# Optimization experiments

Measured on AMD Instinct MI355X. Metric: run time of the kernel, lower is better.

Reference implementation:

```python
import jax, jax.numpy as jnp
import numpy as np

C = 768
H = 12
T = 4096
B = 1
EPS = 1e-5


def setup_inputs() -> dict:
    key = jax.random.key(0)
    ks = jax.random.split(key, 16)
    s = 0.02
    return {
        "x": jax.random.normal(ks[0], (B, T, C), jnp.float32),
        "ln1_w": jnp.ones((C,), jnp.float32),
        "ln1_b": jnp.zeros((C,), jnp.float32),
        "W_attn": jax.random.normal(ks[1], (C, 3 * C), jnp.float32) * s,
        "b_attn": jnp.zeros((3 * C,), jnp.float32),
        "W_proj": jax.random.normal(ks[2], (C, C), jnp.float32) * s,
        "b_proj": jnp.zeros((C,), jnp.float32),
        "ln2_w": jnp.ones((C,), jnp.float32),
        "ln2_b": jnp.zeros((C,), jnp.float32),
        "W_fc": jax.random.normal(ks[3], (C, 4 * C), jnp.float32) * s,
        "b_fc": jnp.zeros((4 * C,), jnp.float32),
        "W_fc2": jax.random.normal(ks[4], (4 * C, C), jnp.float32) * s,
        "b_fc2": jnp.zeros((C,), jnp.float32),
    }


def _layernorm(x, w, b):
    mu = jnp.mean(x, axis=-1, keepdims=True)
    var = jnp.var(x, axis=-1, keepdims=True)
    return (x - mu) * jax.lax.rsqrt(var + EPS) * w + b


def _attn(x, W_attn, b_attn, W_proj, b_proj):
    Bb, Tt, Cc = x.shape
    hd = Cc // H
    qkv = x @ W_attn + b_attn                       # (B,T,3C)
    q, k, v = jnp.split(qkv, 3, axis=-1)
    q = q.reshape(Bb, Tt, H, hd).transpose(0, 2, 1, 3)  # (B,H,T,hd)
    k = k.reshape(Bb, Tt, H, hd).transpose(0, 2, 1, 3)
    v = v.reshape(Bb, Tt, H, hd).transpose(0, 2, 1, 3)
    att = jnp.einsum('bhqd,bhkd->bhqk', q, k) * (1.0 / np.sqrt(hd))
    causal = jnp.tril(jnp.ones((Tt, Tt), bool))
    att = jnp.where(causal, att, -jnp.inf)
    att = jax.nn.softmax(att, axis=-1)
    y = jnp.einsum('bhqk,bhkd->bhqd', att, v)       # (B,H,T,hd)
    y = y.transpose(0, 2, 1, 3).reshape(Bb, Tt, Cc)
    return y @ W_proj + b_proj


def _mlp(x, W_fc, b_fc, W_fc2, b_fc2):
    h = jax.nn.gelu(x @ W_fc + b_fc, approximate=False)
    return h @ W_fc2 + b_fc2


def reference(x, ln1_w, ln1_b, W_attn, b_attn, W_proj, b_proj,
              ln2_w, ln2_b, W_fc, b_fc, W_fc2, b_fc2):
    x = x + _attn(_layernorm(x, ln1_w, ln1_b), W_attn, b_attn, W_proj, b_proj)
    x = x + _mlp(_layernorm(x, ln2_w, ln2_b), W_fc, b_fc, W_fc2, b_fc2)
    return x
```

## Files before the change

kernel.cpp:

```cpp
#include <hip/hip_runtime.h>
#include <hip/hip_bf16.h>
#include <math.h>
#include <type_traits>

#define TSEQ 4096
#define CDIM 768
#define NH 12
#define HD 64

typedef float f32x4 __attribute__((ext_vector_type(4)));
typedef __bf16 bf16x8 __attribute__((ext_vector_type(8)));
typedef short s16x8 __attribute__((ext_vector_type(8)));
typedef uint u32x4 __attribute__((ext_vector_type(4)));
typedef uint u32x2 __attribute__((ext_vector_type(2)));

__device__ inline ushort f2bf(float f) {
  __hip_bfloat16 h = __float2bfloat16(f);
  return __builtin_bit_cast(ushort, h);
}

__device__ inline void async16(const void* g, void* l) {
  __builtin_amdgcn_global_load_lds(
      (__attribute__((address_space(1))) unsigned int*)(uintptr_t)g,
      (__attribute__((address_space(3))) unsigned int*)(uintptr_t)l, 16, 0, 0);
}

__device__ inline float exp2_fast(float x) {
  float r;
  asm volatile("v_exp_f32 %0, %1\n\ts_nop 0" : "=v"(r) : "v"(x));
  return r;
}

__device__ inline uint cvtpk(float a, float b) {
  uint r;
  asm volatile("v_cvt_pk_bf16_f32 %0, %1, %2" : "=v"(r) : "v"(a), "v"(b));
  return r;
}

__device__ inline u32x4 gload16(const void* p) {
  u32x4 r;
  asm volatile("global_load_dwordx4 %0, %1, off" : "=&v"(r) : "v"(p) : "memory");
  return r;
}

__device__ inline bf16x8 frag_read(const ushort* base, int row, int kk, int lane) {
  const int byte = row * 128 + ((((kk * 4 + (lane >> 4)) ^ (row & 7))) << 4);
  return *(const bf16x8*)((const char*)base + byte);
}

__device__ inline bf16x8 frag_readK(const ushort* base, int row, int kk, int g) {
  const int f = ((row & 3) << 1) | ((row >> 3) & 1);
  const int byte = row * 128 + (((kk * 4 + g) ^ f) << 4);
  return *(const bf16x8*)((const char*)base + byte);
}

__device__ void wconv_body(const float* __restrict__ W, ushort* __restrict__ Wt,
                           int K, int N, int bx, int by)
{
  __shared__ float sm[32][33];
  const int n0 = bx * 32, k0 = by * 32;
  const int c = threadIdx.x & 31, r0 = threadIdx.x >> 5;
#pragma unroll
  for (int i = 0; i < 4; ++i) {
    const int r = r0 + i * 8;
    sm[r][c] = W[(size_t)(k0 + r) * N + n0 + c];
  }
  __syncthreads();
#pragma unroll
  for (int i = 0; i < 4; ++i) {
    const int r = r0 + i * 8;
    Wt[(size_t)(n0 + r) * K + k0 + c] = f2bf(sm[c][r]);
  }
}

__device__ void ln_body(const float* __restrict__ x, const float* __restrict__ w,
                        const float* __restrict__ b, ushort* __restrict__ out, int row)
{
  const int tid = threadIdx.x;
  const float* xr = x + (size_t)row * CDIM;
  float v[3];
  float s1 = 0.f, s2 = 0.f;
#pragma unroll
  for (int i = 0; i < 3; ++i) {
    v[i] = xr[tid + i * 256];
    s1 += v[i];
    s2 += v[i] * v[i];
  }
#pragma unroll
  for (int off = 32; off >= 1; off >>= 1) {
    s1 += __shfl_xor(s1, off, 64);
    s2 += __shfl_xor(s2, off, 64);
  }
  __shared__ float red1[4], red2[4];
  if ((tid & 63) == 0) { red1[tid >> 6] = s1; red2[tid >> 6] = s2; }
  __syncthreads();
  s1 = red1[0] + red1[1] + red1[2] + red1[3];
  s2 = red2[0] + red2[1] + red2[2] + red2[3];
  const float mu = s1 * (1.f / CDIM);
  const float var = s2 * (1.f / CDIM) - mu * mu;
  const float inv = rsqrtf(var + 1e-5f);
#pragma unroll
  for (int i = 0; i < 3; ++i) {
    const int c2 = tid + i * 256;
    out[(size_t)row * CDIM + c2] = f2bf((v[i] - mu) * inv * w[c2] + b[c2]);
  }
}

__global__ __launch_bounds__(256) void prep_kernel(
    const float* __restrict__ W_attn, ushort* __restrict__ Wt_attn,
    const float* __restrict__ W_proj, ushort* __restrict__ Wt_proj,
    const float* __restrict__ W_fc,   ushort* __restrict__ Wt_fc,
    const float* __restrict__ W_fc2,  ushort* __restrict__ Wt_fc2,
    const float* __restrict__ x, const float* __restrict__ ln1w,
    const float* __restrict__ ln1b, ushort* __restrict__ t_ln)
{
  int b = blockIdx.x;
  if (b < 1728) { wconv_body(W_attn, Wt_attn, 768, 2304, b % 72, b / 72); return; }
  b -= 1728;
  if (b < 576)  { wconv_body(W_proj, Wt_proj, 768, 768, b % 24, b / 24); return; }
  b -= 576;
  if (b < 2304) { wconv_body(W_fc, Wt_fc, 768, 3072, b % 96, b / 96); return; }
  b -= 2304;
  if (b < 2304) { wconv_body(W_fc2, Wt_fc2, 3072, 768, b % 24, b / 24); return; }
  b -= 2304;
  ln_body(x, ln1w, ln1b, t_ln, b);
}

__global__ __launch_bounds__(256) void ln_kernel(
    const float* __restrict__ x, const float* __restrict__ w,
    const float* __restrict__ b, ushort* __restrict__ out)
{
  ln_body(x, w, b, out, blockIdx.x);
}

template <int EPI, int BN>
__global__ __launch_bounds__(256) void gemm_bt(
    const ushort* __restrict__ A, const ushort* __restrict__ Bt,
    const float* __restrict__ bias, const float* __restrict__ res,
    ushort* __restrict__ outb, float* __restrict__ outf,
    int M, int N, int K, int gx, ushort* __restrict__ vTout)
{
  constexpr int NW = BN / 32;
  __shared__ __align__(16) ushort As[3][128 * 32];
  __shared__ __align__(16) ushort Bs[3][BN * 32];
  const int tid = threadIdx.x;
  const int lane = tid & 63;
  const int wv = tid >> 6;
  const int nwg = (int)gridDim.x;
  const int bid = (int)blockIdx.x;
  const int sw = (bid & 7) * (nwg >> 3) + (bid >> 3);
  const int rowBase = (sw / gx) * 128;
  const int colBase = (sw % gx) * BN;
  const int wr = (wv >> 1) * 64;
  const int wc = (wv & 1) * (BN / 2);

  f32x4 acc[4][NW] = {};

  const int e0 = tid * 8;
  const int r0 = e0 >> 5, c0 = e0 & 31;
  const int e1 = (tid + 256) * 8;
  const int r1 = e1 >> 5, c1 = e1 & 31;

  const ushort* Ag0 = A + (size_t)(rowBase + r0) * K + c0;
  const ushort* Ag1 = A + (size_t)(rowBase + r1) * K + c1;
  const ushort* Bg0 = Bt + (size_t)(colBase + r0) * K + c0;
  const ushort* Bg1 = Bt + (size_t)(colBase + r1) * K + c1;

  auto stage = [&](int buf, int k0) {
    async16(Ag0 + k0, &As[buf][e0]);
    async16(Ag1 + k0, &As[buf][e1]);
    async16(Bg0 + k0, &Bs[buf][e0]);
    if (BN == 128) async16(Bg1 + k0, &Bs[buf][e1]);
  };

  const int nt = K / 32;
  stage(0, 0);
  stage(1, 32);
  int b0 = 0, b1 = 1, b2 = 2;
  for (int t = 0; t < nt; ++t) {
    if (t < nt - 1) {
      if (BN == 128) asm volatile("s_waitcnt vmcnt(4)" ::: "memory");
      else           asm volatile("s_waitcnt vmcnt(3)" ::: "memory");
    } else {
      asm volatile("s_waitcnt vmcnt(0)" ::: "memory");
    }
    __builtin_amdgcn_sched_barrier(0);
    __builtin_amdgcn_s_barrier();
    __builtin_amdgcn_sched_barrier(0);
    if (t + 2 < nt) stage(b2, t * 32 + 64);

    bf16x8 af[4], bfr[NW];
#pragma unroll
    for (int m = 0; m < 4; ++m)
      af[m] = *(const bf16x8*)&As[b0][(wr + m * 16 + (lane & 15)) * 32 + (lane >> 4) * 8];
#pragma unroll
    for (int n = 0; n < NW; ++n)
      bfr[n] = *(const bf16x8*)&Bs[b0][(wc + n * 16 + (lane & 15)) * 32 + (lane >> 4) * 8];
    __builtin_amdgcn_s_setprio(1);
#pragma unroll
    for (int m = 0; m < 4; ++m)
#pragma unroll
      for (int n = 0; n < NW; ++n)
        acc[m][n] = __builtin_amdgcn_mfma_f32_16x16x32_bf16(af[m], bfr[n], acc[m][n], 0, 0, 0);
    __builtin_amdgcn_s_setprio(0);
    const int tmp = b0; b0 = b1; b1 = b2; b2 = tmp;
  }

  if (EPI == 0 && vTout != nullptr && colBase >= 1536) {
#pragma unroll
    for (int n = 0; n < NW; ++n) {
      const int gc = colBase + wc + n * 16 + (lane & 15);
      const float bv = bias[gc];
      const size_t cp = (size_t)(gc - 1536) * 4096;
#pragma unroll
      for (int m = 0; m < 4; ++m) {
        const int gr0 = rowBase + wr + m * 16 + (lane >> 4) * 4;
        u32x2 pk;
        pk.x = cvtpk(acc[m][n][0] + bv, acc[m][n][1] + bv);
        pk.y = cvtpk(acc[m][n][2] + bv, acc[m][n][3] + bv);
        *(u32x2*)&vTout[cp + gr0] = pk;
      }
    }
    return;
  }

#pragma unroll
  for (int n = 0; n < NW; ++n) {
    const int gc = colBase + wc + n * 16 + (lane & 15);
    const float bv = bias[gc];
#pragma unroll
    for (int m = 0; m < 4; ++m) {
#pragma unroll
      for (int j = 0; j < 4; ++j) {
        const int gr = rowBase + wr + m * 16 + (lane >> 4) * 4 + j;
        const float v = acc[m][n][j] + bv;
        if (EPI == 0) {
          outb[(size_t)gr * N + gc] = f2bf(v);
        } else if (EPI == 1) {
          outf[(size_t)gr * N + gc] = res[(size_t)gr * N + gc] + v;
        } else {
          const float g = 0.5f * v * (1.0f + erff(v * 0.70710678118654752f));
          outb[(size_t)gr * N + gc] = f2bf(g);
        }
      }
    }
  }
}

__global__ __launch_bounds__(256) void attn_kernel(
    const ushort* __restrict__ qkv, const ushort* __restrict__ vT,
    ushort* __restrict__ att)
{
  __shared__ __align__(16) char smem[20480];

  const int tid = threadIdx.x;
  const int lane = tid & 63;
  const int wv = tid >> 6;
  const int g = lane >> 4;
  const int ql = lane & 15;
  const int kh = wv & 1;
  const int qh = wv >> 1;
  const int p_ = blockIdx.x & 255, grp = blockIdx.x >> 8;
  const int item = (grp & 1) ? (grp * 256 + 255 - p_) : (grp * 256 + p_);
  const int qb = 63 - (item / 12);
  const int h = item % 12;
  const int t0 = qb * 64;
  const size_t rs = 3 * CDIM;
  const int qo = h * HD, ko = CDIM + h * HD;

  const float cexp = 0.18033688f;
  const float cbias = -32.0f * 0.18033688f;

  const int L0 = tid * 16, L1 = (tid + 256) * 16;
  const int r_0 = L0 >> 7, c_0 = ((L0 >> 4) & 7) ^ (((r_0 & 3) << 1) | ((r_0 >> 3) & 1));
  const int r_1 = L1 >> 7, c_1 = ((L1 >> 4) & 7) ^ (((r_1 & 3) << 1) | ((r_1 >> 3) & 1));
  const ushort* kg0 = qkv + (size_t)r_0 * rs + ko + c_0 * 8;
  const ushort* kg1 = qkv + (size_t)r_1 * rs + ko + c_1 * 8;

  const ushort* vB = vT + (size_t)(h * 64 + ql) * 4096 + 32 * kh + 8 * g;

  bf16x8 qf[2][2];
#pragma unroll
  for (int qg = 0; qg < 2; ++qg) {
    const ushort* qrow = qkv + (size_t)(t0 + 32 * qh + 16 * qg + ql) * rs + qo + g * 8;
    qf[qg][0] = *(const bf16x8*)(qrow);
    qf[qg][1] = *(const bf16x8*)(qrow + 32);
  }

  async16(kg0, smem + L0);
  async16(kg1, smem + L1);

  f32x4 accO[2][4] = {};
  f32x4 accL[2] = {};
  const bf16x8 ones = __builtin_bit_cast(bf16x8,
      (u32x4){0x3F803F80u, 0x3F803F80u, 0x3F803F80u, 0x3F803F80u});

  auto body = [&](int kb, int curb, auto first_c, auto diag_c) {
    constexpr bool FIRST = decltype(first_c)::value;
    constexpr bool DIAG = decltype(diag_c)::value;
    const ushort* Kt = (const ushort*)(smem + curb * 8192);

    u32x4 vfr[4];
#pragma unroll
    for (int n = 0; n < 4; ++n)
      vfr[n] = gload16(vB + (size_t)kb * 64 + (size_t)n * 16 * 4096);

    if (FIRST) asm volatile("s_waitcnt vmcnt(0)" ::: "memory");
    else       asm volatile("s_waitcnt vmcnt(4)" ::: "memory");
    __builtin_amdgcn_sched_barrier(0);
    __builtin_amdgcn_s_barrier();
    __builtin_amdgcn_sched_barrier(0);

    if (!DIAG) {
      const size_t koff = (size_t)(kb + 1) * 64 * rs;
      async16(kg0 + koff, smem + (curb ^ 1) * 8192 + L0);
      async16(kg1 + koff, smem + (curb ^ 1) * 8192 + L1);
    }

    f32x4 accS[2][2] = {};
    __builtin_amdgcn_s_setprio(1);
#pragma unroll
    for (int kg = 0; kg < 2; ++kg)
#pragma unroll
      for (int kk = 0; kk < 2; ++kk) {
        const bf16x8 A = frag_readK(Kt, 32 * kh + 8 * (ql >> 2) + 4 * kg + (ql & 3), kk, g);
#pragma unroll
        for (int qg = 0; qg < 2; ++qg)
          accS[kg][qg] = __builtin_amdgcn_mfma_f32_16x16x32_bf16(
              A, qf[qg][kk], accS[kg][qg], 0, 0, 0);
      }
    __builtin_amdgcn_s_setprio(0);

    bf16x8 pa[2];
#pragma unroll
    for (int qg = 0; qg < 2; ++qg) {
      float e[2][4];
#pragma unroll
      for (int kg = 0; kg < 2; ++kg)
#pragma unroll
        for (int j = 0; j < 4; ++j) {
          float s = exp2_fast(fmaf(accS[kg][qg][j], cexp, cbias));
          if (DIAG && (32 * kh + 8 * g + 4 * kg + j) > (32 * qh + 16 * qg + ql)) s = 0.f;
          e[kg][j] = s;
        }
      const uint w0 = cvtpk(e[0][0], e[0][1]);
      const uint w1 = cvtpk(e[0][2], e[0][3]);
      const uint w2 = cvtpk(e[1][0], e[1][1]);
      const uint w3 = cvtpk(e[1][2], e[1][3]);
      pa[qg] = __builtin_bit_cast(bf16x8, (u32x4){w0, w1, w2, w3});
    }

    if (DIAG) asm volatile("s_waitcnt vmcnt(0)" ::: "memory");
    else      asm volatile("s_waitcnt vmcnt(2)" ::: "memory");
    __builtin_amdgcn_sched_barrier(0);

    __builtin_amdgcn_s_setprio(1);
#pragma unroll
    for (int n = 0; n < 4; ++n) {
      const bf16x8 bv = __builtin_bit_cast(bf16x8, vfr[n]);
#pragma unroll
      for (int qg = 0; qg < 2; ++qg)
        accO[qg][n] = __builtin_amdgcn_mfma_f32_16x16x32_bf16(pa[qg], bv, accO[qg][n], 0, 0, 0);
    }
#pragma unroll
    for (int qg = 0; qg < 2; ++qg)
      accL[qg] = __builtin_amdgcn_mfma_f32_16x16x32_bf16(pa[qg], ones, accL[qg], 0, 0, 0);
    __builtin_amdgcn_s_setprio(0);
  };

  if (qb == 0) {
    body(0, 0, std::true_type{}, std::true_type{});
  } else {
    body(0, 0, std::true_type{}, std::false_type{});
    int cur = 1;
    for (int kb = 1; kb < qb; ++kb) {
      body(kb, cur, std::false_type{}, std::false_type{});
      cur ^= 1;
    }
    body(qb, cur, std::false_type{}, std::true_type{});
  }

  __syncthreads();
  float* mO = (float*)smem;
  float* mL = (float*)(smem + 16384);
  if (kh == 1) {
#pragma unroll
    for (int qg = 0; qg < 2; ++qg) {
#pragma unroll
      for (int n = 0; n < 4; ++n)
        *(f32x4*)&mO[(((qh * 2 + qg) * 4 + n) * 64 + lane) * 4] = accO[qg][n];
      *(f32x4*)&mL[((qh * 2 + qg) * 64 + lane) * 4] = accL[qg];
    }
  }
  __syncthreads();
  if (kh == 0) {
#pragma unroll
    for (int qg = 0; qg < 2; ++qg) {
      const f32x4 ls = accL[qg] + *(const f32x4*)&mL[((qh * 2 + qg) * 64 + lane) * 4];
      f32x4 inv4;
#pragma unroll
      for (int jr = 0; jr < 4; ++jr) inv4[jr] = 1.0f / ls[jr];
#pragma unroll
      for (int n = 0; n < 4; ++n) {
        const f32x4 o = accO[qg][n] +
            *(const f32x4*)&mO[(((qh * 2 + qg) * 4 + n) * 64 + lane) * 4];
#pragma unroll
        for (int jr = 0; jr < 4; ++jr) {
          const int tq = t0 + 32 * qh + 16 * qg + 4 * g + jr;
          const int d = 16 * n + ql;
          att[(size_t)tq * CDIM + h * HD + d] = f2bf(o[jr] * inv4[jr]);
        }
      }
    }
  }
}

extern "C" void kernel_launch(void* const* d_in, const int* in_sizes, int n_in,
                              void* d_out, int out_size, void* d_ws, size_t ws_size,
                              hipStream_t stream)
{
  const float* x      = (const float*)d_in[0];
  const float* ln1_w  = (const float*)d_in[1];
  const float* ln1_b  = (const float*)d_in[2];
  const float* W_attn = (const float*)d_in[3];
  const float* b_attn = (const float*)d_in[4];
  const float* W_proj = (const float*)d_in[5];
  const float* b_proj = (const float*)d_in[6];
  const float* ln2_w  = (const float*)d_in[7];
  const float* ln2_b  = (const float*)d_in[8];
  const float* W_fc   = (const float*)d_in[9];
  const float* b_fc   = (const float*)d_in[10];
  const float* W_fc2  = (const float*)d_in[11];
  const float* b_fc2  = (const float*)d_in[12];
  float* out = (float*)d_out;

  char* base = (char*)d_ws;
  size_t off = 0;
  auto alloc = [&](size_t bytes) -> void* {
    void* q = base + off;
    off = (off + bytes + 255) & ~(size_t)255;
    return q;
  };
  ushort* Wt_attn = (ushort*)alloc(768ull * 2304 * 2);
  ushort* Wt_proj = (ushort*)alloc(768ull * 768 * 2);
  ushort* Wt_fc   = (ushort*)alloc(768ull * 3072 * 2);
  ushort* Wt_fc2  = (ushort*)alloc(3072ull * 768 * 2);
  ushort* t_ln    = (ushort*)alloc(4096ull * 768 * 2);
  ushort* t_att   = (ushort*)alloc(4096ull * 768 * 2);
  float*  t_x1    = (float*) alloc(4096ull * 768 * 4);
  ushort* t_big   = (ushort*)alloc(4096ull * 3072 * 2);
  ushort* t_qkv = t_big;
  ushort* t_vT  = t_big + 4096ull * 2304;
  ushort* t_h   = t_big;

  prep_kernel<<<11008, 256, 0, stream>>>(
      W_attn, Wt_attn, W_proj, Wt_proj, W_fc, Wt_fc, W_fc2, Wt_fc2,
      x, ln1_w, ln1_b, t_ln);
  gemm_bt<0, 128><<<18 * 32, 256, 0, stream>>>(
      t_ln, Wt_attn, b_attn, nullptr, t_qkv, nullptr, 4096, 2304, 768, 18, t_vT);
  attn_kernel<<<dim3(768), 256, 0, stream>>>(t_qkv, t_vT, t_att);
  gemm_bt<1, 64><<<12 * 32, 256, 0, stream>>>(
      t_att, Wt_proj, b_proj, x, nullptr, t_x1, 4096, 768, 768, 12, nullptr);
  ln_kernel<<<4096, 256, 0, stream>>>(t_x1, ln2_w, ln2_b, t_ln);
  gemm_bt<2, 128><<<24 * 32, 256, 0, stream>>>(
      t_ln, Wt_fc, b_fc, nullptr, t_h, nullptr, 4096, 3072, 768, 24, nullptr);
  gemm_bt<1, 64><<<12 * 32, 256, 0, stream>>>(
      t_h, Wt_fc2, b_fc2, t_x1, nullptr, out, 4096, 768, 3072, 12, nullptr);
}
```

Measured before the change: 195.5 us.

## Give each attention wave a private K tile buffer to drop block barriers

Each of the four waves now stages its own 32-row slice of the K tile into a private double-buffered LDS region, so the per-iteration block-wide s_barrier is removed and waves sync only through their own vmcnt waits. Q fragments are loaded with explicit async global loads that overlap the first K staging. The LDS footprint grows from 20 KB to 32 KB, which may lower occupancy. The vmcnt accounting is reworked to match the new count of outstanding loads.

Result: no change. 199.1 us (+1.8%).

```diff
diff --git a/kernel.cpp b/kernel.cpp
--- a/kernel.cpp
+++ b/kernel.cpp
@@ -48,10 +48,10 @@
   return *(const bf16x8*)((const char*)base + byte);
 }
 
-__device__ inline bf16x8 frag_readK(const ushort* base, int row, int kk, int g) {
-  const int f = ((row & 3) << 1) | ((row >> 3) & 1);
-  const int byte = row * 128 + (((kk * 4 + g) ^ f) << 4);
-  return *(const bf16x8*)((const char*)base + byte);
+__device__ inline bf16x8 frag_readKw(const char* base, int lr, int kk, int g) {
+  const int f = ((lr & 3) << 1) | ((lr >> 3) & 1);
+  const int byte = lr * 128 + (((kk * 4 + g) ^ f) << 4);
+  return *(const bf16x8*)(base + byte);
 }
 
 __device__ void wconv_body(const float* __restrict__ W, ushort* __restrict__ Wt,
@@ -251,7 +251,7 @@
     const ushort* __restrict__ qkv, const ushort* __restrict__ vT,
     ushort* __restrict__ att)
 {
-  __shared__ __align__(16) char smem[20480];
+  __shared__ __align__(16) char smem[32768];
 
   const int tid = threadIdx.x;
   const int lane = tid & 63;
@@ -271,51 +271,56 @@
   const float cexp = 0.18033688f;
   const float cbias = -32.0f * 0.18033688f;
 
-  const int L0 = tid * 16, L1 = (tid + 256) * 16;
-  const int r_0 = L0 >> 7, c_0 = ((L0 >> 4) & 7) ^ (((r_0 & 3) << 1) | ((r_0 >> 3) & 1));
-  const int r_1 = L1 >> 7, c_1 = ((L1 >> 4) & 7) ^ (((r_1 & 3) << 1) | ((r_1 >> 3) & 1));
-  const ushort* kg0 = qkv + (size_t)r_0 * rs + ko + c_0 * 8;
-  const ushort* kg1 = qkv + (size_t)r_1 * rs + ko + c_1 * 8;
+  char* wbase = smem + wv * 8192;
+
+  const ushort* kgsrc = qkv + (size_t)(32 * kh + (lane >> 3)) * rs + ko;
+  const int schunk0 = (lane & 7) ^ (((lane >> 3) & 3) << 1);
 
   const ushort* vB = vT + (size_t)(h * 64 + ql) * 4096 + 32 * kh + 8 * g;
 
+  const ushort* qrow0 = qkv + (size_t)(t0 + 32 * qh + ql) * rs + qo + g * 8;
+  u32x4 qraw[4];
+  qraw[0] = gload16(qrow0);
+  qraw[1] = gload16(qrow0 + 32);
+  qraw[2] = gload16(qrow0 + 16 * rs);
+  qraw[3] = gload16(qrow0 + 16 * rs + 32);
+
+  auto stageK = [&](int buf, int kb) {
+#pragma unroll
+    for (int i = 0; i < 4; ++i) {
+      const ushort* src = kgsrc + ((size_t)kb * 64 + 8 * i) * rs + (schunk0 ^ (i & 1)) * 8;
+      async16(src, wbase + buf * 4096 + i * 1024 + lane * 16);
+    }
+  };
+
+  stageK(0, 0);
+  asm volatile("s_waitcnt vmcnt(4)" ::: "memory");
+  __builtin_amdgcn_sched_barrier(0);
   bf16x8 qf[2][2];
-#pragma unroll
-  for (int qg = 0; qg < 2; ++qg) {
-    const ushort* qrow = qkv + (size_t)(t0 + 32 * qh + 16 * qg + ql) * rs + qo + g * 8;
-    qf[qg][0] = *(const bf16x8*)(qrow);
-    qf[qg][1] = *(const bf16x8*)(qrow + 32);
-  }
-
-  async16(kg0, smem + L0);
-  async16(kg1, smem + L1);
+  qf[0][0] = __builtin_bit_cast(bf16x8, qraw[0]);
+  qf[0][1] = __builtin_bit_cast(bf16x8, qraw[1]);
+  qf[1][0] = __builtin_bit_cast(bf16x8, qraw[2]);
+  qf[1][1] = __builtin_bit_cast(bf16x8, qraw[3]);
 
   f32x4 accO[2][4] = {};
   f32x4 accL[2] = {};
   const bf16x8 ones = __builtin_bit_cast(bf16x8,
       (u32x4){0x3F803F80u, 0x3F803F80u, 0x3F803F80u, 0x3F803F80u});
 
-  auto body = [&](int kb, int curb, auto first_c, auto diag_c) {
-    constexpr bool FIRST = decltype(first_c)::value;
+  auto body = [&](int kb, int curb, auto diag_c) {
     constexpr bool DIAG = decltype(diag_c)::value;
-    const ushort* Kt = (const ushort*)(smem + curb * 8192);
+    const char* Kt = wbase + curb * 4096;
 
     u32x4 vfr[4];
 #pragma unroll
     for (int n = 0; n < 4; ++n)
       vfr[n] = gload16(vB + (size_t)kb * 64 + (size_t)n * 16 * 4096);
 
-    if (FIRST) asm volatile("s_waitcnt vmcnt(0)" ::: "memory");
+    if (!DIAG) stageK(curb ^ 1, kb + 1);
+
+    if (!DIAG) asm volatile("s_waitcnt vmcnt(8)" ::: "memory");
     else       asm volatile("s_waitcnt vmcnt(4)" ::: "memory");
     __builtin_amdgcn_sched_barrier(0);
-    __builtin_amdgcn_s_barrier();
-    __builtin_amdgcn_sched_barrier(0);
-
-    if (!DIAG) {
-      const size_t koff = (size_t)(kb + 1) * 64 * rs;
-      async16(kg0 + koff, smem + (curb ^ 1) * 8192 + L0);
-      async16(kg1 + koff, smem + (curb ^ 1) * 8192 + L1);
-    }
 
     f32x4 accS[2][2] = {};
     __builtin_amdgcn_s_setprio(1);
@@ -323,7 +328,7 @@
     for (int kg = 0; kg < 2; ++kg)
 #pragma unroll
       for (int kk = 0; kk < 2; ++kk) {
-        const bf16x8 A = frag_readK(Kt, 32 * kh + 8 * (ql >> 2) + 4 * kg + (ql & 3), kk, g);
+        const bf16x8 A = frag_readKw(Kt, 8 * (ql >> 2) + 4 * kg + (ql & 3), kk, g);
 #pragma unroll
         for (int qg = 0; qg < 2; ++qg)
           accS[kg][qg] = __builtin_amdgcn_mfma_f32_16x16x32_bf16(
@@ -350,8 +355,8 @@
       pa[qg] = __builtin_bit_cast(bf16x8, (u32x4){w0, w1, w2, w3});
     }
 
-    if (DIAG) asm volatile("s_waitcnt vmcnt(0)" ::: "memory");
-    else      asm volatile("s_waitcnt vmcnt(2)" ::: "memory");
+    if (!DIAG) asm volatile("s_waitcnt vmcnt(4)" ::: "memory");
+    else       asm volatile("s_waitcnt vmcnt(0)" ::: "memory");
     __builtin_amdgcn_sched_barrier(0);
 
     __builtin_amdgcn_s_setprio(1);
@@ -368,17 +373,12 @@
     __builtin_amdgcn_s_setprio(0);
   };
 
-  if (qb == 0) {
-    body(0, 0, std::true_type{}, std::true_type{});
-  } else {
-    body(0, 0, std::true_type{}, std::false_type{});
-    int cur = 1;
-    for (int kb = 1; kb < qb; ++kb) {
-      body(kb, cur, std::false_type{}, std::false_type{});
-      cur ^= 1;
-    }
-    body(qb, cur, std::false_type{}, std::true_type{});
-  }
+  int cur = 0;
+  for (int kb = 0; kb < qb; ++kb) {
+    body(kb, cur, std::false_type{});
+    cur ^= 1;
+  }
+  body(qb, cur, std::true_type{});
 
   __syncthreads();
   float* mO = (float*)smem;
```

## Split attention block across 8 waves with one 16-row query group each

Applied to the files above, without the earlier changes.

The attention kernel now runs with 512 threads per block: each of 8 waves handles 16 query rows instead of 32, so per-wave accumulators and MFMA work halve. The K tile load is split across twice as many threads, with one async load each, and the wait counts change to match. The block still covers 64 queries. This is meant to raise wave-level parallelism and hide latency, at the cost of more barrier participants and V loads repeated per wave.

After: 239.4 us. 1.22x slower.

```diff
diff --git a/kernel.cpp b/kernel.cpp
--- a/kernel.cpp
+++ b/kernel.cpp
@@ -41,11 +41,6 @@
   u32x4 r;
   asm volatile("global_load_dwordx4 %0, %1, off" : "=&v"(r) : "v"(p) : "memory");
   return r;
-}
-
-__device__ inline bf16x8 frag_read(const ushort* base, int row, int kk, int lane) {
-  const int byte = row * 128 + ((((kk * 4 + (lane >> 4)) ^ (row & 7))) << 4);
-  return *(const bf16x8*)((const char*)base + byte);
 }
 
 __device__ inline bf16x8 frag_readK(const ushort* base, int row, int kk, int g) {
@@ -247,7 +242,7 @@
   }
 }
 
-__global__ __launch_bounds__(256) void attn_kernel(
+__global__ __launch_bounds__(512) void attn_kernel(
     const ushort* __restrict__ qkv, const ushort* __restrict__ vT,
     ushort* __restrict__ att)
 {
@@ -271,32 +266,28 @@
   const float cexp = 0.18033688f;
   const float cbias = -32.0f * 0.18033688f;
 
-  const int L0 = tid * 16, L1 = (tid + 256) * 16;
-  const int r_0 = L0 >> 7, c_0 = ((L0 >> 4) & 7) ^ (((r_0 & 3) << 1) | ((r_0 >> 3) & 1));
-  const int r_1 = L1 >> 7, c_1 = ((L1 >> 4) & 7) ^ (((r_1 & 3) << 1) | ((r_1 >> 3) & 1));
-  const ushort* kg0 = qkv + (size_t)r_0 * rs + ko + c_0 * 8;
-  const ushort* kg1 = qkv + (size_t)r_1 * rs + ko + c_1 * 8;
+  const int L = tid * 16;
+  const int r_ = L >> 7;
+  const int c_ = ((L >> 4) & 7) ^ (((r_ & 3) << 1) | ((r_ >> 3) & 1));
+  const ushort* kg = qkv + (size_t)r_ * rs + ko + c_ * 8;
 
   const ushort* vB = vT + (size_t)(h * 64 + ql) * 4096 + 32 * kh + 8 * g;
 
-  bf16x8 qf[2][2];
-#pragma unroll
-  for (int qg = 0; qg < 2; ++qg) {
-    const ushort* qrow = qkv + (size_t)(t0 + 32 * qh + 16 * qg + ql) * rs + qo + g * 8;
-    qf[qg][0] = *(const bf16x8*)(qrow);
-    qf[qg][1] = *(const bf16x8*)(qrow + 32);
-  }
-
-  async16(kg0, smem + L0);
-  async16(kg1, smem + L1);
-
-  f32x4 accO[2][4] = {};
-  f32x4 accL[2] = {};
+  bf16x8 qf[2];
+  {
+    const ushort* qrow = qkv + (size_t)(t0 + 16 * qh + ql) * rs + qo + g * 8;
+    qf[0] = *(const bf16x8*)(qrow);
+    qf[1] = *(const bf16x8*)(qrow + 32);
+  }
+
+  async16(kg, smem + L);
+
+  f32x4 accO[4] = {};
+  f32x4 accL = {};
   const bf16x8 ones = __builtin_bit_cast(bf16x8,
       (u32x4){0x3F803F80u, 0x3F803F80u, 0x3F803F80u, 0x3F803F80u});
 
-  auto body = [&](int kb, int curb, auto first_c, auto diag_c) {
-    constexpr bool FIRST = decltype(first_c)::value;
+  auto body = [&](int kb, int curb, auto diag_c) {
     constexpr bool DIAG = decltype(diag_c)::value;
     const ushort* Kt = (const ushort*)(smem + curb * 8192);
 
@@ -305,79 +296,65 @@
     for (int n = 0; n < 4; ++n)
       vfr[n] = gload16(vB + (size_t)kb * 64 + (size_t)n * 16 * 4096);
 
-    if (FIRST) asm volatile("s_waitcnt vmcnt(0)" ::: "memory");
-    else       asm volatile("s_waitcnt vmcnt(4)" ::: "memory");
+    asm volatile("s_waitcnt vmcnt(4)" ::: "memory");
     __builtin_amdgcn_sched_barrier(0);
     __builtin_amdgcn_s_barrier();
     __builtin_amdgcn_sched_barrier(0);
 
     if (!DIAG) {
       const size_t koff = (size_t)(kb + 1) * 64 * rs;
-      async16(kg0 + koff, smem + (curb ^ 1) * 8192 + L0);
-      async16(kg1 + koff, smem + (curb ^ 1) * 8192 + L1);
-    }
-
-    f32x4 accS[2][2] = {};
+      async16(kg + koff, smem + (curb ^ 1) * 8192 + L);
+    }
+
+    f32x4 accS[2] = {};
     __builtin_amdgcn_s_setprio(1);
 #pragma unroll
-    for (int kg = 0; kg < 2; ++kg)
+    for (int kg2 = 0; kg2 < 2; ++kg2)
 #pragma unroll
       for (int kk = 0; kk < 2; ++kk) {
-        const bf16x8 A = frag_readK(Kt, 32 * kh + 8 * (ql >> 2) + 4 * kg + (ql & 3), kk, g);
-#pragma unroll
-        for (int qg = 0; qg < 2; ++qg)
-          accS[kg][qg] = __builtin_amdgcn_mfma_f32_16x16x32_bf16(
-              A, qf[qg][kk], accS[kg][qg], 0, 0, 0);
+        const bf16x8 A = frag_readK(Kt, 32 * kh + 8 * (ql >> 2) + 4 * kg2 + (ql & 3), kk, g);
+        accS[kg2] = __builtin_amdgcn_mfma_f32_16x16x32_bf16(A, qf[kk], accS[kg2], 0, 0, 0);
       }
     __builtin_amdgcn_s_setprio(0);
 
-    bf16x8 pa[2];
-#pragma unroll
-    for (int qg = 0; qg < 2; ++qg) {
-      float e[2][4];
-#pragma unroll
-      for (int kg = 0; kg < 2; ++kg)
-#pragma unroll
-        for (int j = 0; j < 4; ++j) {
-          float s = exp2_fast(fmaf(accS[kg][qg][j], cexp, cbias));
-          if (DIAG && (32 * kh + 8 * g + 4 * kg + j) > (32 * qh + 16 * qg + ql)) s = 0.f;
-          e[kg][j] = s;
-        }
-      const uint w0 = cvtpk(e[0][0], e[0][1]);
-      const uint w1 = cvtpk(e[0][2], e[0][3]);
-      const uint w2 = cvtpk(e[1][0], e[1][1]);
-      const uint w3 = cvtpk(e[1][2], e[1][3]);
-      pa[qg] = __builtin_bit_cast(bf16x8, (u32x4){w0, w1, w2, w3});
-    }
+    float e[2][4];
+#pragma unroll
+    for (int kg2 = 0; kg2 < 2; ++kg2)
+#pragma unroll
+      for (int j = 0; j < 4; ++j) {
+        float s = exp2_fast(fmaf(accS[kg2][j], cexp, cbias));
+        if (DIAG && (32 * kh + 8 * g + 4 * kg2 + j) > (16 * qh + ql)) s = 0.f;
+        e[kg2][j] = s;
+      }
+    const uint w0 = cvtpk(e[0][0], e[0][1]);
+    const uint w1 = cvtpk(e[0][2], e[0][3]);
+    const uint w2 = cvtpk(e[1][0], e[1][1]);
+    const uint w3 = cvtpk(e[1][2], e[1][3]);
+    const bf16x8 pa = __builtin_bit_cast(bf16x8, (u32x4){w0, w1, w2, w3});
 
     if (DIAG) asm volatile("s_waitcnt vmcnt(0)" ::: "memory");
-    else      asm volatile("s_waitcnt vmcnt(2)" ::: "memory");
+    else      asm volatile("s_waitcnt vmcnt(1)" ::: "memory");
     __builtin_amdgcn_sched_barrier(0);
 
     __builtin_amdgcn_s_setprio(1);
 #pragma unroll
     for (int n = 0; n < 4; ++n) {
       const bf16x8 bv = __builtin_bit_cast(bf16x8, vfr[n]);
-#pragma unroll
-      for (int qg = 0; qg < 2; ++qg)
-        accO[qg][n] = __builtin_amdgcn_mfma_f32_16x16x32_bf16(pa[qg], bv, accO[qg][n], 0, 0, 0);
-    }
-#pragma unroll
-    for (int qg = 0; qg < 2; ++qg)
-      accL[qg] = __builtin_amdgcn_mfma_f32_16x16x32_bf16(pa[qg], ones, accL[qg], 0, 0, 0);
+      accO[n] = __builtin_amdgcn_mfma_f32_16x16x32_bf16(pa, bv, accO[n], 0, 0, 0);
+    }
+    accL = __builtin_amdgcn_mfma_f32_16x16x32_bf16(pa, ones, accL, 0, 0, 0);
     __builtin_amdgcn_s_setprio(0);
   };
 
   if (qb == 0) {
-    body(0, 0, std::true_type{}, std::true_type{});
+    body(0, 0, std::true_type{});
   } else {
-    body(0, 0, std::true_type{}, std::false_type{});
-    int cur = 1;
-    for (int kb = 1; kb < qb; ++kb) {
-      body(kb, cur, std::false_type{}, std::false_type{});
+    int cur = 0;
+    for (int kb = 0; kb < qb; ++kb) {
+      body(kb, cur, std::false_type{});
       cur ^= 1;
     }
-    body(qb, cur, std::false_type{}, std::true_type{});
+    body(qb, cur, std::true_type{});
   }
 
   __syncthreads();
@@ -385,31 +362,24 @@
   float* mL = (float*)(smem + 16384);
   if (kh == 1) {
 #pragma unroll
-    for (int qg = 0; qg < 2; ++qg) {
-#pragma unroll
-      for (int n = 0; n < 4; ++n)
-        *(f32x4*)&mO[(((qh * 2 + qg) * 4 + n) * 64 + lane) * 4] = accO[qg][n];
-      *(f32x4*)&mL[((qh * 2 + qg) * 64 + lane) * 4] = accL[qg];
-    }
+    for (int n = 0; n < 4; ++n)
+      *(f32x4*)&mO[((qh * 4 + n) * 64 + lane) * 4] = accO[n];
+    *(f32x4*)&mL[(qh * 64 + lane) * 4] = accL;
   }
   __syncthreads();
   if (kh == 0) {
-#pragma unroll
-    for (int qg = 0; qg < 2; ++qg) {
-      const f32x4 ls = accL[qg] + *(const f32x4*)&mL[((qh * 2 + qg) * 64 + lane) * 4];
-      f32x4 inv4;
-#pragma unroll
-      for (int jr = 0; jr < 4; ++jr) inv4[jr] = 1.0f / ls[jr];
-#pragma unroll
-      for (int n = 0; n < 4; ++n) {
-        const f32x4 o = accO[qg][n] +
-            *(const f32x4*)&mO[(((qh * 2 + qg) * 4 + n) * 64 + lane) * 4];
-#pragma unroll
-        for (int jr = 0; jr < 4; ++jr) {
-          const int tq = t0 + 32 * qh + 16 * qg + 4 * g + jr;
-          const int d = 16 * n + ql;
-          att[(size_t)tq * CDIM + h * HD + d] = f2bf(o[jr] * inv4[jr]);
-        }
+    const f32x4 ls = accL + *(const f32x4*)&mL[(qh * 64 + lane) * 4];
+    f32x4 inv4;
+#pragma unroll
+    for (int jr = 0; jr < 4; ++jr) inv4[jr] = 1.0f / ls[jr];
+#pragma unroll
+    for (int n = 0; n < 4; ++n) {
+      const f32x4 o = accO[n] + *(const f32x4*)&mO[((qh * 4 + n) * 64 + lane) * 4];
+#pragma unroll
+      for (int jr = 0; jr < 4; ++jr) {
+        const int tq = t0 + 16 * qh + 4 * g + jr;
+        const int d = 16 * n + ql;
+        att[(size_t)tq * CDIM + h * HD + d] = f2bf(o[jr] * inv4[jr]);
       }
     }
   }
@@ -458,7 +428,7 @@
       x, ln1_w, ln1_b, t_ln);
   gemm_bt<0, 128><<<18 * 32, 256, 0, stream>>>(
       t_ln, Wt_attn, b_attn, nullptr, t_qkv, nullptr, 4096, 2304, 768, 18, t_vT);
-  attn_kernel<<<dim3(768), 256, 0, stream>>>(t_qkv, t_vT, t_att);
+  attn_kernel<<<dim3(768), 512, 0, stream>>>(t_qkv, t_vT, t_att);
   gemm_bt<1, 64><<<12 * 32, 256, 0, stream>>>(
       t_att, Wt_proj, b_proj, x, nullptr, t_x1, 4096, 768, 768, 12, nullptr);
   ln_kernel<<<4096, 256, 0, stream>>>(t_x1, ln2_w, ln2_b, t_ln);
```
